# Kernel optimization log

Measured on AMD Instinct MI355X. Metric: run time of the kernel, lower is better.

The kernel has to match this reference:

```python
import jax, jax.numpy as jnp
import numpy as np

MIN = 1e-15
EPS = 1e-6

# ---- Poincare-ball (c=1) helpers (hyrnn-style MobiusGRU / MobiusLinear) ----

def _artanh(x):
    x = jnp.clip(x, -1 + 1e-7, 1 - 1e-7)
    return 0.5 * (jnp.log1p(x) - jnp.log1p(-x))

def _norm(x):
    return jnp.sqrt(jnp.maximum(jnp.sum(x * x, -1, keepdims=True), MIN))

def m_add(x, y):
    x2 = jnp.sum(x * x, -1, keepdims=True)
    y2 = jnp.sum(y * y, -1, keepdims=True)
    xy = jnp.sum(x * y, -1, keepdims=True)
    num = (1 + 2 * xy + y2) * x + (1 - x2) * y
    den = 1 + 2 * xy + x2 * y2
    return num / jnp.maximum(den, MIN)

def m_matvec(M, x):
    xn = _norm(x)
    mx = x @ M.T
    mxn = _norm(mx)
    return jnp.tanh(mxn / xn * _artanh(xn)) * mx / mxn

def m_pw(w, x):
    xn = _norm(x)
    mx = w * x
    mxn = _norm(mx)
    return jnp.tanh(mxn / xn * _artanh(xn)) * mx / mxn

def logmap0(x):
    xn = _norm(x)
    return _artanh(xn) * x / xn

def one_transform(W, h, U, x, b):
    return m_add(m_add(m_matvec(W, h), m_matvec(U, x)), b)

def mobius_gru(xs, Wih, Whh, b):
    # xs: [S, B, I]; Wih/Whh: [3, H, *]; b: [3, H]; chunk order (r, h, z)
    def step(h, x):
        z = jax.nn.sigmoid(logmap0(one_transform(Whh[2], h, Wih[2], x, b[2])))
        r = jax.nn.sigmoid(logmap0(one_transform(Whh[0], h, Wih[0], x, b[0])))
        rh = m_pw(r, h)
        htil = one_transform(Whh[1], rh, Wih[1], x, b[1])
        hn = m_add(h, m_pw(z, m_add(-h, htil)))
        return hn, hn
    h0 = jnp.zeros((xs.shape[1], Whh.shape[1]), xs.dtype)
    _, ys = jax.lax.scan(step, h0, xs)
    return ys

# ---- Lorentz-model helpers ----

def arcosh(x):
    return jnp.log(x) + jnp.log1p(jnp.sqrt(jnp.maximum(x * x - 1 + EPS, 0.0)) / x)

def lorentz_activation(x):
    r = jnp.sqrt(jnp.sum(x * x, -1, keepdims=True))
    return jnp.concatenate([x / r * jnp.sinh(r), jnp.cosh(r)], -1)

def lorentz_to_klein(x):
    return x[..., :-1] / jnp.clip(x[..., -1:], EPS, 1e16)

def poincare_to_lorentz(x):
    r2 = jnp.sum(x * x, -1, keepdims=True)
    return jnp.concatenate([2 * x, 1 + r2], -1) / (1 - r2 + EPS)

# ---- HyperbolicPostAttention ----

def post_attention(x, Wih_f, Whh_f, b_f, Wih_b, Whh_b, b_b, centroid, Wp, bp, beta):
    # x: [L, 100]
    x = x / jnp.sqrt(1 + jnp.sum(x * x, -1, keepdims=True))
    S = x.shape[0] // 100
    f1 = mobius_gru(x.reshape(S, 100, 100), Wih_f, Whh_f, b_f)
    f2 = mobius_gru(x[::-1].reshape(S, 100, 100), Wih_b, Whh_b, b_b)
    f = jnp.concatenate([f1, f2], -1)                       # [S,100,200]
    out_k = lorentz_to_klein(poincare_to_lorentz(f))        # [S,100,200]
    att = m_add(m_matvec(Wp, f), bp)                        # MobiusLinear
    att_l = poincare_to_lorentz(att)                        # [S,100,201]
    cent = lorentz_activation(centroid[None, None, :])      # [1,1,201]
    prod = att_l * cent
    pm = jnp.clip(-jnp.sum(prod[..., :-1], -1) + prod[..., -1], 1.0 + EPS, 1e16)
    a = -beta * arcosh(pm) - 1.0                            # [S,100]; c=1.0
    e = jnp.exp(a - a.max())
    inv_gamma = 1 - jnp.sum(out_k * out_k, -1)
    gamma = jnp.clip(1 / jnp.sqrt(jnp.clip(inv_gamma, EPS, 1 - EPS)), 1 + EPS, 1e16)
    r = e * gamma
    r = r / jnp.sum(r, axis=0)
    o = jnp.einsum('sb,sbd->sd', r, out_k)                  # [S,200]
    return o / (1 + jnp.sqrt(1 + jnp.sum(o * o, -1, keepdims=True)))


def setup_inputs() -> dict:
    key = jax.random.key(0)
    ks = jax.random.split(key, 16)
    n = lambda k, s, sd: jax.random.normal(k, s, jnp.float32) * sd
    return {
        'x_': n(ks[0], (16, 2000, 768), 1.0),
        'W1': n(ks[1], (100, 768), 0.02), 'b1': n(ks[2], (100,), 0.02),
        'W2': n(ks[3], (768, 200), 0.02), 'b2': n(ks[4], (768,), 0.02),
        'Wih_f': n(ks[5], (3, 100, 100), 0.02), 'Whh_f': n(ks[6], (3, 100, 100), 0.02),
        'bias_f': n(ks[7], (3, 100), 0.01),
        'Wih_b': n(ks[8], (3, 100, 100), 0.02), 'Whh_b': n(ks[9], (3, 100, 100), 0.02),
        'bias_b': n(ks[10], (3, 100), 0.01),
        'centroid': n(ks[11], (200,), 0.05),
        'Wp': n(ks[12], (200, 200), 0.02), 'bp': n(ks[13], (200,), 0.01),
        'beta': n(ks[14], (1,), 0.05),
    }


def reference(x_, W1, b1, W2, b2, Wih_f, Whh_f, bias_f, Wih_b, Whh_b, bias_b,
              centroid, Wp, bp, beta):
    xk = lorentz_to_klein(lorentz_activation(x_))           # [N,L,768]

    def per(x):
        h = x @ W1.T + b1                                   # [L,100]
        s = post_attention(h, Wih_f, Whh_f, bias_f, Wih_b, Whh_b, bias_b,
                           centroid, Wp, bp, beta)          # [S,200]
        return s @ W2.T + b2                                # [S,768]

    return jnp.squeeze(jax.vmap(per)(xk))                   # [N,S,768]
```

## Files before the change

### kernel.cpp

```cpp
#include <hip/hip_runtime.h>
#include <hip/hip_bf16.h>

#define MINF 1e-15f
#define EPSF 1e-6f

#define OFF_P    0u
#define OFF_UX   3200000u
#define OFF_WT4  22400000u
#define OFF_F    22460000u
#define OFF_CL   28860000u
#define OFF_A    28860256u
#define OFF_G    28892256u
#define OFF_WGT  28924256u
#define OFF_WI4  OFF_F
#define OFF_W1P  (OFF_F + 60000u)
#define OFF_MX   OFF_UX
#define OFF_WP4  OFF_A
#define OFF_NUB  OFF_P

#define K3_LDS_BYTES ((30000 + 2*13*112) * 4)
#define K2_LDS_BYTES ((3200 + 64*26)*16 + 64*4)
#define K4G_LDS_BYTES ((3200 + 64*26)*16)

__device__ __forceinline__ float wred(float v) {
#pragma unroll
  for (int m = 32; m > 0; m >>= 1) v += __shfl_xor(v, m, 64);
  return v;
}
__device__ __forceinline__ float wredmax(float v) {
#pragma unroll
  for (int m = 32; m > 0; m >>= 1) v = fmaxf(v, __shfl_xor(v, m, 64));
  return v;
}

__device__ __forceinline__ float rcp_(float x) { return __builtin_amdgcn_rcpf(x); }
__device__ __forceinline__ float sqrt_(float x) { return __builtin_amdgcn_sqrtf(x); }
__device__ __forceinline__ float rsq_(float x) { return __builtin_amdgcn_rsqf(x); }
__device__ __forceinline__ float tanh_f(float y) {
  if (y > 15.f) return 1.f;
  float y2 = y * y;
  if (y < 0.1f) return y * (1.f - y2 * (1.f / 3.f) + y2 * y2 * (2.f / 15.f));
  float e = __expf(2.f * y);
  return (e - 1.f) * rcp_(e + 1.f);
}
__device__ __forceinline__ float artanh_ov(float x) {
  x = fminf(x, 1.f - 1e-7f);
  float x2 = x * x;
  if (x < 0.1f) return 1.f + x2 * (1.f / 3.f) + x2 * x2 * 0.2f;
  return 0.5f * __logf((1.f + x) * rcp_(1.f - x)) * rcp_(x);
}
__device__ __forceinline__ float sigm_f(float x) { return rcp_(1.f + __expf(-x)); }
__device__ __forceinline__ float arcosh_(float x) {
  return logf(x) + log1pf(sqrtf(fmaxf(x * x - 1.f + EPSF, 0.f)) / x);
}

__global__ void k0_pack(const float* __restrict__ whh_f, const float* __restrict__ whh_b,
                        const float* __restrict__ wih_f, const float* __restrict__ wih_b,
                        const float* __restrict__ W1, const float* __restrict__ Wp,
                        const float* __restrict__ centroid,
                        float* __restrict__ wt4, float* __restrict__ wi4,
                        float* __restrict__ w1p, float* __restrict__ wp4,
                        float* __restrict__ cl) {
  __shared__ float sred[4];
  if (blockIdx.x == 925) {
    int t = threadIdx.x;
    float v = (t < 200) ? centroid[t] : 0.f;
    float ps = wred(v * v);
    if ((t & 63) == 0) sred[t >> 6] = ps;
    __syncthreads();
    float r = sqrtf(sred[0] + sred[1] + sred[2] + sred[3]);
    if (t < 200) cl[t] = v / r * sinhf(r);
    if (t == 0) cl[200] = coshf(r);
    return;
  }
  int idx = blockIdx.x * 256 + threadIdx.x;
  if (idx < 60000) {
    int kk = idx & 3; int t = idx >> 2;
    int j = t % 100; t /= 100;
    int k4 = t % 25; t /= 25;
    int g = t % 3; int dir = t / 3;
    const float* src = dir ? whh_b : whh_f;
    wt4[idx] = src[g * 10000 + j * 100 + k4 * 4 + kk];
  } else if (idx < 120000) {
    int i2 = idx - 60000;
    int kk = i2 & 3; int t = i2 >> 2;
    int c = t % 100; t /= 100;
    int k4 = t % 25; t /= 25;
    int g = t % 3; int dir = t / 3;
    const float* src = dir ? wih_b : wih_f;
    wi4[i2] = src[g * 10000 + c * 100 + k4 * 4 + kk];
  } else if (idx < 196800) {
    int i2 = idx - 120000;
    int kk = i2 & 3; int t = i2 >> 2;
    int c = t % 100; int k4 = t / 100;
    w1p[i2] = W1[c * 768 + k4 * 4 + kk];
  } else if (idx < 236800) {
    int i3 = idx - 196800;
    int kk = i3 & 3; int t = i3 >> 2;
    int c = t % 100; int t2 = t / 100;
    int k4 = t2 % 50; int ch = t2 / 50;
    wp4[i3] = Wp[(size_t)(ch * 100 + c) * 200 + k4 * 4 + kk];
  }
}

__global__ __launch_bounds__(256, 2) void k1(const float* __restrict__ x_,
                                             const float* __restrict__ w1p,
                                             const float* __restrict__ b1,
                                             float* __restrict__ p) {
  __shared__ float4 wl[16 * 128];
  __shared__ float4 xl[64 * 16];
  __shared__ float ns[64];
  __shared__ float sscale[64];
  int t = threadIdx.x;
  int row0 = blockIdx.x * 64;
  int cg = t & 31, rg = t >> 5;
  const float4* wsrc = (const float4*)w1p;
  float nacc[4] = {0, 0, 0, 0};
  float acc[8][4] = {};
  for (int kc = 0; kc < 12; kc++) {
    int k0f4 = kc * 16;
    __syncthreads();
#pragma unroll
    for (int q = 0; q < 4; q++) {
      int idx = t + 256 * q;
      int r = idx >> 4, c4 = idx & 15;
      float4 v = *(const float4*)(x_ + (size_t)(row0 + r) * 768 + (size_t)(k0f4 + c4) * 4);
      xl[idx] = v;
      nacc[q] += v.x * v.x + v.y * v.y + v.z * v.z + v.w * v.w;
    }
#pragma unroll
    for (int q = 0; q < 8; q++) {
      int idx = t + 256 * q;
      int k4 = idx >> 7, c = idx & 127;
      float4 v = {0, 0, 0, 0};
      if (c < 100) v = wsrc[(size_t)(k0f4 + k4) * 100 + c];
      wl[idx] = v;
    }
    __syncthreads();
#pragma unroll 4
    for (int k4 = 0; k4 < 16; k4++) {
      float4 wv[4];
#pragma unroll
      for (int j = 0; j < 4; j++) wv[j] = wl[k4 * 128 + cg + 32 * j];
#pragma unroll
      for (int i = 0; i < 8; i++) {
        float4 pv = xl[(rg * 8 + i) * 16 + k4];
#pragma unroll
        for (int j = 0; j < 4; j++)
          acc[i][j] += pv.x * wv[j].x + pv.y * wv[j].y + pv.z * wv[j].z + pv.w * wv[j].w;
      }
    }
  }
  __syncthreads();
#pragma unroll
  for (int q = 0; q < 4; q++) {
    float v = nacc[q];
#pragma unroll
    for (int m = 8; m > 0; m >>= 1) v += __shfl_xor(v, m, 64);
    if ((t & 15) == 0) ns[(t >> 4) + 16 * q] = v;
  }
  __syncthreads();
  if (t < 64) {
    float rr = sqrt_(fmaxf(ns[t], MINF));
    sscale[t] = tanh_f(rr) * rcp_(rr);
  }
  __syncthreads();
  float bcol[4];
#pragma unroll
  for (int j = 0; j < 4; j++) {
    int col = cg + 32 * j;
    bcol[j] = (col < 100) ? b1[col] : 0.f;
  }
#pragma unroll
  for (int i = 0; i < 8; i++) {
    int r = rg * 8 + i;
    float s = sscale[r];
    float hv[4]; float ss = 0.f;
#pragma unroll
    for (int j = 0; j < 4; j++) {
      int col = cg + 32 * j;
      hv[j] = (col < 100) ? (s * acc[i][j] + bcol[j]) : 0.f;
      ss += hv[j] * hv[j];
    }
#pragma unroll
    for (int m = 16; m > 0; m >>= 1) ss += __shfl_xor(ss, m, 64);
    float inv = rsq_(1.f + ss);
    float* prow = p + (size_t)(row0 + r) * 100;
#pragma unroll
    for (int j = 0; j < 4; j++) {
      int col = cg + 32 * j;
      if (col < 100) prow[col] = hv[j] * inv;
    }
  }
}

__global__ __launch_bounds__(256, 2) void k2(const float* __restrict__ p,
                                             const float* __restrict__ wi4,
                                             float* __restrict__ ux) {
  extern __shared__ float4 l4[];
  float4* wl = l4;
  float4* pl = l4 + 3200;
  float* alx = (float*)(l4 + 3200 + 64 * 26);
  int t = threadIdx.x;
  int bx = blockIdx.x;
  int combo = bx / 500, tile = bx % 500;
  int row0 = tile * 64;
  int cg = t & 31, rg = t >> 5;
  const float4* wsrc = (const float4*)wi4 + (size_t)combo * 2500;
#pragma unroll
  for (int q = 0; q < 13; q++) {
    int idx = t + 256 * q;
    if (idx < 3200) {
      int k4 = idx >> 7, c = idx & 127;
      float4 v = {0, 0, 0, 0};
      if (c < 100) v = wsrc[k4 * 100 + c];
      wl[idx] = v;
    }
  }
  const float4* psrc = (const float4*)(p + (size_t)row0 * 100);
#pragma unroll
  for (int q = 0; q < 7; q++) {
    int idx = t + 256 * q;
    if (idx < 1600) {
      int r = idx / 25, c4 = idx % 25;
      pl[r * 26 + c4] = psrc[idx];
    }
  }
  __syncthreads();
  {
    int w = t >> 6, lane = t & 63;
    const float* pf = (const float*)pl;
    for (int r = w * 16; r < w * 16 + 16; r++) {
      float v0 = pf[r * 104 + lane];
      float v1 = (lane < 36) ? pf[r * 104 + 64 + lane] : 0.f;
      float s2 = wred(v0 * v0 + v1 * v1);
      if (lane == 0) {
        float xn = sqrt_(fmaxf(s2, MINF));
        alx[r] = artanh_ov(xn);
      }
    }
  }
  __syncthreads();
  float acc[8][4] = {};
#pragma unroll 5
  for (int k4 = 0; k4 < 25; k4++) {
    float4 wv[4];
#pragma unroll
    for (int j = 0; j < 4; j++) wv[j] = wl[k4 * 128 + cg + 32 * j];
#pragma unroll
    for (int i = 0; i < 8; i++) {
      float4 pv = pl[(rg * 8 + i) * 26 + k4];
#pragma unroll
      for (int j = 0; j < 4; j++)
        acc[i][j] += pv.x * wv[j].x + pv.y * wv[j].y + pv.z * wv[j].z + pv.w * wv[j].w;
    }
  }
#pragma unroll
  for (int i = 0; i < 8; i++) {
    int r = rg * 8 + i;
    float ss = acc[i][0] * acc[i][0] + acc[i][1] * acc[i][1] +
               acc[i][2] * acc[i][2] + acc[i][3] * acc[i][3];
#pragma unroll
    for (int m = 16; m > 0; m >>= 1) ss += __shfl_xor(ss, m, 64);
    float mxn = sqrt_(fmaxf(ss, MINF));
    float sc = tanh_f(mxn * alx[r]) * rcp_(mxn);
    float* dst = ux + ((size_t)combo * 32000 + row0 + r) * 100;
#pragma unroll
    for (int j = 0; j < 4; j++) {
      int col = cg + 32 * j;
      if (col < 100) dst[col] = sc * acc[i][j];
    }
  }
}

__global__ __launch_bounds__(256) void k2b(const float* __restrict__ ux,
                                           const float* __restrict__ bias_f,
                                           const float* __restrict__ bias_b,
                                           float* __restrict__ nub) {
  int t = threadIdx.x; int w = t >> 6; int lane = t & 63;
  int gr0 = blockIdx.x * 64;
  int combo = gr0 / 32000;
  int dir = combo / 3, g = combo % 3;
  const float* bias = (dir ? bias_b : bias_f) + g * 100;
  float b0 = bias[lane];
  float b1 = (lane < 36) ? bias[64 + lane] : 0.f;
  for (int i = w * 16; i < w * 16 + 16; i++) {
    const float* u = ux + (size_t)(gr0 + i) * 100;
    float u0 = u[lane];
    float u1 = (lane < 36) ? u[64 + lane] : 0.f;
    float n2 = wred(u0 * u0 + u1 * u1);
    float ub = wred(u0 * b0 + u1 * b1);
    if (lane == 0) { nub[gr0 + i] = n2; nub[192000 + gr0 + i] = ub; }
  }
}

__device__ __forceinline__ void mv100x2_reg(const float* __restrict__ Wz,
                                            const float* __restrict__ Wr,
                                            const float* __restrict__ hrow,
                                            int lane, bool hi,
                                            float& mz0, float& mz1,
                                            float& mr0, float& mr1) {
  const float4* Wz4 = (const float4*)Wz;
  const float4* Wr4 = (const float4*)Wr;
  const float4* h4 = (const float4*)hrow;
  float4 az0 = {0, 0, 0, 0}, az1 = {0, 0, 0, 0};
  float4 ar0 = {0, 0, 0, 0}, ar1 = {0, 0, 0, 0};
#pragma unroll 5
  for (int k4 = 0; k4 < 25; k4++) {
    float4 hv = h4[k4];
    float4 wz = Wz4[k4 * 100 + lane];
    float4 wr = Wr4[k4 * 100 + lane];
    az0.x += wz.x * hv.x; az0.y += wz.y * hv.y; az0.z += wz.z * hv.z; az0.w += wz.w * hv.w;
    ar0.x += wr.x * hv.x; ar0.y += wr.y * hv.y; ar0.z += wr.z * hv.z; ar0.w += wr.w * hv.w;
    if (hi) {
      float4 wzh = Wz4[k4 * 100 + 64 + lane];
      float4 wrh = Wr4[k4 * 100 + 64 + lane];
      az1.x += wzh.x * hv.x; az1.y += wzh.y * hv.y; az1.z += wzh.z * hv.z; az1.w += wzh.w * hv.w;
      ar1.x += wrh.x * hv.x; ar1.y += wrh.y * hv.y; ar1.z += wrh.z * hv.z; ar1.w += wrh.w * hv.w;
    }
  }
  mz0 = az0.x + az0.y + az0.z + az0.w;
  mr0 = ar0.x + ar0.y + ar0.z + ar0.w;
  mz1 = az1.x + az1.y + az1.z + az1.w;
  mr1 = ar1.x + ar1.y + ar1.z + ar1.w;
}

__device__ __forceinline__ void mv100_reg(const float* __restrict__ Wg,
                                          const float* __restrict__ hrow,
                                          int lane, bool hi,
                                          float& m0, float& m1) {
  const float4* W4 = (const float4*)Wg;
  const float4* h4 = (const float4*)hrow;
  float4 a0 = {0, 0, 0, 0}, a1 = {0, 0, 0, 0};
#pragma unroll 5
  for (int k4 = 0; k4 < 25; k4++) {
    float4 hv = h4[k4];
    float4 w0 = W4[k4 * 100 + lane];
    a0.x += w0.x * hv.x; a0.y += w0.y * hv.y; a0.z += w0.z * hv.z; a0.w += w0.w * hv.w;
    if (hi) {
      float4 w1 = W4[k4 * 100 + 64 + lane];
      a1.x += w1.x * hv.x; a1.y += w1.y * hv.y; a1.z += w1.z * hv.z; a1.w += w1.w * hv.w;
    }
  }
  m0 = a0.x + a0.y + a0.z + a0.w;
  m1 = a1.x + a1.y + a1.z + a1.w;
}

__device__ __forceinline__ void gate_ot(float m0, float m1, float u0, float u1,
                                        float b0v, float b1v, float C, float ub, float nb2,
                                        float alphah,
                                        float& c0, float& c1, float& Fout) {
  float A = wred(m0 * m0 + m1 * m1);
  float B = wred(m0 * u0 + m1 * u1);
  float Mb = wred(m0 * b0v + m1 * b1v);
  float mxn = sqrt_(fmaxf(A, MINF));
  float gam = tanh_f(mxn * alphah) * rcp_(mxn);
  float x2 = gam * gam * A, xy = gam * B;
  float rd = rcp_(fmaxf(1.f + 2.f * xy + x2 * C, MINF));
  float cA = (1.f + 2.f * xy + C) * gam * rd, cB = (1.f - x2) * rd;
  float D = fmaxf(cA * cA * A + 2.f * cA * cB * B + cB * cB * C, 0.f);
  float E = cA * Mb + cB * ub;
  float r2 = rcp_(fmaxf(1.f + 2.f * E + D * nb2, MINF));
  float t1 = (1.f + 2.f * E + nb2) * r2, t2 = (1.f - D) * r2;
  c0 = t1 * (cA * m0 + cB * u0) + t2 * b0v;
  c1 = t1 * (cA * m1 + cB * u1) + t2 * b1v;
  Fout = fmaxf(t1 * t1 * D + 2.f * t1 * t2 * E + t2 * t2 * nb2, MINF);
}

__global__ __launch_bounds__(1024, 1) void k3(const float* __restrict__ ux,
                                              const float* __restrict__ nub,
                                              const float* __restrict__ wt4,
                                              const float* __restrict__ bias_f,
                                              const float* __restrict__ bias_b,
                                              float* __restrict__ f) {
  extern __shared__ float lds[];
  float* Wlds = lds;
  float* hl = lds + 30000;
  float* rhl = hl + 13 * 112;
  int t = threadIdx.x; int w = t >> 6; int lane = t & 63;
  bool hi = lane < 36;
  int bx = blockIdx.x;
  int grp = bx >> 3; int blki = bx & 7;
  int n = grp >> 1; int dir = grp & 1;
  int b0 = blki * 13; int nrows = min(13, 100 - b0);
  const float* bias = dir ? bias_b : bias_f;
  const float4* wsrc4 = (const float4*)(wt4 + dir * 30000);
  float4* Wlds4 = (float4*)Wlds;
#pragma unroll
  for (int q = 0; q < 8; q++) { int idx = t + 1024 * q; if (idx < 7500) Wlds4[idx] = wsrc4[idx]; }
  int row = w; bool erow = (w < nrows);
  if (erow) {
    hl[row * 112 + lane] = 0.f;
    if (hi) hl[row * 112 + 64 + lane] = 0.f;
  }
  __syncthreads();
  if (!erow) return;

  int b = b0 + row;
  float nh2 = 0.f, h0 = 0.f, h1 = 0.f;
  float br0 = bias[lane],       br1 = hi ? bias[64 + lane] : 0.f;
  float bh0 = bias[100 + lane], bh1 = hi ? bias[164 + lane] : 0.f;
  float bz0 = bias[200 + lane], bz1 = hi ? bias[264 + lane] : 0.f;
  float nbr2 = wred(br0 * br0 + br1 * br1);
  float nbh2 = wred(bh0 * bh0 + bh1 * bh1);
  float nbz2 = wred(bz0 * bz0 + bz1 * bz1);

  for (int s = 0; s < 20; s++) {
    float mz0, mz1, mr0, mr1;
    mv100x2_reg(Wlds + 2 * 10000, Wlds + 0 * 10000, hl + row * 112, lane, hi,
                mz0, mz1, mr0, mr1);
    int l = dir ? (1999 - (s * 100 + b)) : (s * 100 + b);
    size_t rowg = (size_t)n * 2000 + l;
    size_t iz = (size_t)(dir * 3 + 2) * 32000 + rowg;
    size_t ir = (size_t)(dir * 3 + 0) * 32000 + rowg;
    size_t ih = (size_t)(dir * 3 + 1) * 32000 + rowg;
    const float* uxz = ux + iz * 100;
    const float* uxr = ux + ir * 100;
    const float* uxhp = ux + ih * 100;
    float uz0 = uxz[lane],  uz1 = hi ? uxz[lane + 64] : 0.f;
    float ur0 = uxr[lane],  ur1 = hi ? uxr[lane + 64] : 0.f;
    float uxh0 = uxhp[lane], uxh1 = hi ? uxhp[lane + 64] : 0.f;
    float Cz = nub[iz], ubz = nub[192000 + iz];
    float Cr = nub[ir], ubr = nub[192000 + ir];
    float Ch = nub[ih], ubh = nub[192000 + ih];
    float xnh = sqrt_(fmaxf(nh2, MINF));
    float alphah = artanh_ov(xnh);
    float cz0, cz1, Fz, cr0, cr1, Fr;
    gate_ot(mz0, mz1, uz0, uz1, bz0, bz1, Cz, ubz, nbz2, alphah, cz0, cz1, Fz);
    gate_ot(mr0, mr1, ur0, ur1, br0, br1, Cr, ubr, nbr2, alphah, cr0, cr1, Fr);
    float lgz = artanh_ov(sqrt_(Fz));
    float z0 = sigm_f(lgz * cz0), z1 = sigm_f(lgz * cz1);
    float lgr = artanh_ov(sqrt_(Fr));
    float rg0 = sigm_f(lgr * cr0), rg1 = sigm_f(lgr * cr1);
    float mx0 = rg0 * h0, mx1 = rg1 * h1;
    float G = wred(mx0 * mx0 + mx1 * mx1);
    float mxnr = sqrt_(fmaxf(G, MINF));
    float srh = tanh_f(mxnr * alphah) * rcp_(mxnr);
    rhl[row * 112 + lane] = srh * mx0;
    if (hi) rhl[row * 112 + lane + 64] = srh * mx1;
    float nrh2 = srh * srh * G;
    float mh0, mh1;
    mv100_reg(Wlds + 1 * 10000, rhl + row * 112, lane, hi, mh0, mh1);
    float xnrh = sqrt_(fmaxf(nrh2, MINF));
    float alpharh = artanh_ov(xnrh);
    float ct0, ct1, T;
    gate_ot(mh0, mh1, uxh0, uxh1, bh0, bh1, Ch, ubh, nbh2, alpharh, ct0, ct1, T);
    float U = wred(h0 * ct0 + h1 * ct1);
    float rdd = rcp_(fmaxf(1.f - 2.f * U + nh2 * T, MINF));
    float cAd = (1.f - 2.f * U + T) * rdd, cBd = (1.f - nh2) * rdd;
    float d0 = -cAd * h0 + cBd * ct0, d1 = -cAd * h1 + cBd * ct1;
    float nd2 = fmaxf(cAd * cAd * nh2 - 2.f * cAd * cBd * U + cBd * cBd * T, MINF);
    float zd0 = z0 * d0, zd1 = z1 * d1;
    float P = wred(zd0 * zd0 + zd1 * zd1);
    float Q = wred(h0 * zd0 + h1 * zd1);
    float xnd = sqrt_(nd2);
    float mxnp = sqrt_(fmaxf(P, MINF));
    float sp = tanh_f(mxnp * artanh_ov(xnd)) * rcp_(mxnp);
    float y2p = sp * sp * P, xyp = sp * Q;
    float r3 = rcp_(fmaxf(1.f + 2.f * xyp + nh2 * y2p, MINF));
    float A1 = (1.f + 2.f * xyp + y2p) * r3, B1 = (1.f - nh2) * r3 * sp;
    float hn0 = A1 * h0 + B1 * zd0, hn1 = A1 * h1 + B1 * zd1;
    nh2 = fmaxf(A1 * A1 * nh2 + 2.f * A1 * B1 * Q + B1 * B1 * P, 0.f);
    h0 = hn0; h1 = hn1;
    hl[row * 112 + lane] = hn0;
    if (hi) hl[row * 112 + lane + 64] = hn1;
    float* fd = f + (((size_t)n * 20 + s) * 100 + b) * 200 + dir * 100;
    fd[lane] = hn0;
    if (hi) fd[lane + 64] = hn1;
  }
}

__global__ __launch_bounds__(256, 2) void k4ag(const float* __restrict__ f,
                                               const float* __restrict__ wp4,
                                               float* __restrict__ mx) {
  extern __shared__ float4 g4[];
  float4* wl = g4;
  float4* pl = g4 + 3200;
  int t = threadIdx.x;
  int bx = blockIdx.x;
  int ch = bx & 1, tile = bx >> 1;
  int row0 = tile * 64;
  int cg = t & 31, rg = t >> 5;
  const float4* wsrc = (const float4*)wp4 + (size_t)ch * 5000;
  const float4* psrc = (const float4*)(f + (size_t)row0 * 200);
  float acc[8][4] = {};
  for (int kc = 0; kc < 2; kc++) {
    __syncthreads();
#pragma unroll
    for (int q = 0; q < 13; q++) {
      int idx = t + 256 * q;
      if (idx < 3200) {
        int k4 = idx >> 7, c = idx & 127;
        float4 v = {0, 0, 0, 0};
        if (c < 100) v = wsrc[(kc * 25 + k4) * 100 + c];
        wl[idx] = v;
      }
    }
#pragma unroll
    for (int q = 0; q < 7; q++) {
      int idx = t + 256 * q;
      if (idx < 1600) {
        int r = idx / 25, k4 = idx % 25;
        pl[r * 26 + k4] = psrc[r * 50 + kc * 25 + k4];
      }
    }
    __syncthreads();
#pragma unroll 5
    for (int k4 = 0; k4 < 25; k4++) {
      float4 wv[4];
#pragma unroll
      for (int j = 0; j < 4; j++) wv[j] = wl[k4 * 128 + cg + 32 * j];
#pragma unroll
      for (int i = 0; i < 8; i++) {
        float4 pv = pl[(rg * 8 + i) * 26 + k4];
#pragma unroll
        for (int j = 0; j < 4; j++)
          acc[i][j] += pv.x * wv[j].x + pv.y * wv[j].y + pv.z * wv[j].z + pv.w * wv[j].w;
      }
    }
  }
#pragma unroll
  for (int i = 0; i < 8; i++) {
    float* dst = mx + (size_t)(row0 + rg * 8 + i) * 200 + ch * 100;
#pragma unroll
    for (int j = 0; j < 4; j++) {
      int col = cg + 32 * j;
      if (col < 100) dst[col] = acc[i][j];
    }
  }
}

__global__ __launch_bounds__(256) void k4ae(const float* __restrict__ f,
                                            const float* __restrict__ mx,
                                            const float* __restrict__ bp,
                                            const float* __restrict__ cl,
                                            const float* __restrict__ beta_p,
                                            float* __restrict__ a_out, float* __restrict__ g_out) {
  int t = threadIdx.x; int w = t >> 6; int lane = t & 63;
  int row0 = blockIdx.x * 64;
  float beta = beta_p[0];
  float c200 = cl[200];
  float b_0 = bp[lane], b_1 = bp[lane + 64], b_2 = bp[lane + 128];
  float b_3 = (lane < 8) ? bp[lane + 192] : 0.f;
  float c_0 = cl[lane], c_1 = cl[lane + 64], c_2 = cl[lane + 128];
  float c_3 = (lane < 8) ? cl[lane + 192] : 0.f;
  float nbp2 = wred(b_0 * b_0 + b_1 * b_1 + b_2 * b_2 + b_3 * b_3);
  for (int r = w * 16; r < w * 16 + 16; r++) {
    const float* fr = f + (size_t)(row0 + r) * 200;
    const float* mr = mx + (size_t)(row0 + r) * 200;
    float f0 = fr[lane], f1 = fr[lane + 64], f2 = fr[lane + 128];
    float f3 = (lane < 8) ? fr[lane + 192] : 0.f;
    float nf2 = wred(f0 * f0 + f1 * f1 + f2 * f2 + f3 * f3);
    float xn = sqrt_(fmaxf(nf2, MINF));
    float alx = artanh_ov(xn);
    float m0 = mr[lane], m1 = mr[lane + 64], m2 = mr[lane + 128];
    float m3 = (lane < 8) ? mr[lane + 192] : 0.f;
    float A = wred(m0 * m0 + m1 * m1 + m2 * m2 + m3 * m3);
    float B = wred(m0 * b_0 + m1 * b_1 + m2 * b_2 + m3 * b_3);
    float mxn = sqrt_(fmaxf(A, MINF));
    float gam = tanh_f(mxn * alx) * rcp_(mxn);
    float x2 = gam * gam * A, y2 = nbp2, xy = gam * B;
    float rd = rcp_(fmaxf(1.f + 2.f * xy + x2 * y2, MINF));
    float cA = (1.f + 2.f * xy + y2) * gam * rd, cB = (1.f - x2) * rd;
    float a0 = cA * m0 + cB * b_0, a1 = cA * m1 + cB * b_1;
    float a2 = cA * m2 + cB * b_2, a3 = cA * m3 + cB * b_3;
    float r2 = wred(a0 * a0 + a1 * a1 + a2 * a2 + a3 * a3);
    float dc = wred(a0 * c_0 + a1 * c_1 + a2 * c_2 + a3 * c_3);
    float pm = (-2.f * dc + (1.f + r2) * c200) / (1.f - r2 + EPSF);
    pm = fminf(fmaxf(pm, 1.f + EPSF), 1e16f);
    float av = -beta * arcosh_(pm) - 1.f;
    float invg = 1.f - 4.f * nf2 / ((1.f + nf2) * (1.f + nf2));
    invg = fminf(fmaxf(invg, EPSF), 1.f - EPSF);
    float gv = fminf(fmaxf(rsq_(invg), 1.f + EPSF), 1e16f);
    if (lane == 0) { a_out[row0 + r] = av; g_out[row0 + r] = gv; }
  }
}

__global__ __launch_bounds__(256) void k4b(const float* __restrict__ a_in,
                                           const float* __restrict__ g_in,
                                           float* __restrict__ wgt) {
  __shared__ float rl[2000];
  __shared__ float sred[4];
  __shared__ float rsinv[100];
  int n = blockIdx.x; int t = threadIdx.x;
  int w = t >> 6, lane = t & 63;
  const float* ap = a_in + n * 2000;
  const float* gp = g_in + n * 2000;
  float av[8]; float am = -1e30f;
#pragma unroll
  for (int q = 0; q < 8; q++) {
    int i = t + 256 * q;
    av[q] = (i < 2000) ? ap[i] : -1e30f;
    am = fmaxf(am, av[q]);
  }
  am = wredmax(am);
  if (lane == 0) sred[w] = am;
  __syncthreads();
  float amax = fmaxf(fmaxf(sred[0], sred[1]), fmaxf(sred[2], sred[3]));
#pragma unroll
  for (int q = 0; q < 8; q++) {
    int i = t + 256 * q;
    if (i < 2000) rl[i] = expf(av[q] - amax) * gp[i];
  }
  __syncthreads();
  if (t < 100) {
    float ssum = 0.f;
#pragma unroll
    for (int s = 0; s < 20; s++) ssum += rl[s * 100 + t];
    rsinv[t] = 1.f / ssum;
  }
  __syncthreads();
#pragma unroll
  for (int q = 0; q < 8; q++) {
    int i = t + 256 * q;
    if (i < 2000) wgt[n * 2000 + i] = rl[i] * rsinv[i % 100];
  }
}

__global__ __launch_bounds__(256) void k4c(const float* __restrict__ f, const float* __restrict__ wgt,
                                           const float* __restrict__ W2, const float* __restrict__ b2,
                                           float* __restrict__ out) {
  __shared__ float cw[100];
  __shared__ float part[4][204];
  __shared__ float ol[200];
  __shared__ float sred[4];
  int bx = blockIdx.x; int n = bx / 20, s = bx % 20;
  int t = threadIdx.x; int w = t >> 6; int lane = t & 63;
  const float* fb = f + ((size_t)n * 20 + s) * 100 * 200;
  for (int bi = w * 25; bi < w * 25 + 25; bi++) {
    const float* fr = fb + bi * 200;
    float v0 = fr[lane], v1 = fr[lane + 64], v2 = fr[lane + 128];
    float v3 = (lane < 8) ? fr[lane + 192] : 0.f;
    float s2 = wred(v0 * v0 + v1 * v1 + v2 * v2 + v3 * v3);
    if (lane == 0) cw[bi] = wgt[n * 2000 + s * 100 + bi] * 2.f * rcp_(1.f + s2);
  }
  __syncthreads();
  float o0 = 0, o1 = 0, o2 = 0, o3 = 0;
  for (int bi = w * 25; bi < w * 25 + 25; bi++) {
    float c = cw[bi];
    const float* fr = fb + bi * 200;
    o0 += c * fr[lane]; o1 += c * fr[lane + 64]; o2 += c * fr[lane + 128];
    if (lane < 8) o3 += c * fr[lane + 192];
  }
  part[w][lane] = o0; part[w][lane + 64] = o1; part[w][lane + 128] = o2;
  if (lane < 8) part[w][lane + 192] = o3;
  __syncthreads();
  float o = 0.f;
  if (t < 200) o = part[0][t] + part[1][t] + part[2][t] + part[3][t];
  float ps = (t < 200) ? o * o : 0.f;
  ps = wred(ps);
  if (lane == 0) sred[w] = ps;
  __syncthreads();
  float no2 = sred[0] + sred[1] + sred[2] + sred[3];
  float denom = 1.f + sqrtf(1.f + no2);
  if (t < 200) ol[t] = o / denom;
  __syncthreads();
  const float4* ol4 = (const float4*)ol;
#pragma unroll
  for (int jj = 0; jj < 3; jj++) {
    int j = t + 256 * jj;
    const float4* wrow = (const float4*)(W2 + (size_t)j * 200);
    float a0 = 0, a1 = 0, a2 = 0, a3 = 0;
    for (int k4 = 0; k4 < 50; k4++) {
      float4 wv = wrow[k4]; float4 ov = ol4[k4];
      a0 += wv.x * ov.x; a1 += wv.y * ov.y; a2 += wv.z * ov.z; a3 += wv.w * ov.w;
    }
    out[((size_t)n * 20 + s) * 768 + j] = a0 + a1 + a2 + a3 + b2[j];
  }
}

extern "C" void kernel_launch(void* const* d_in, const int* in_sizes, int n_in,
                              void* d_out, int out_size, void* d_ws, size_t ws_size,
                              hipStream_t stream) {
  const float* x_     = (const float*)d_in[0];
  const float* W1     = (const float*)d_in[1];
  const float* b1     = (const float*)d_in[2];
  const float* W2     = (const float*)d_in[3];
  const float* b2     = (const float*)d_in[4];
  const float* Wih_f  = (const float*)d_in[5];
  const float* Whh_f  = (const float*)d_in[6];
  const float* bias_f = (const float*)d_in[7];
  const float* Wih_b  = (const float*)d_in[8];
  const float* Whh_b  = (const float*)d_in[9];
  const float* bias_b = (const float*)d_in[10];
  const float* centroid = (const float*)d_in[11];
  const float* Wp     = (const float*)d_in[12];
  const float* bp     = (const float*)d_in[13];
  const float* beta   = (const float*)d_in[14];
  float* out = (float*)d_out;
  float* ws = (float*)d_ws;
  float* p   = ws + OFF_P;
  float* ux  = ws + OFF_UX;
  float* wt4 = ws + OFF_WT4;
  float* f   = ws + OFF_F;
  float* wi4 = ws + OFF_WI4;
  float* w1p = ws + OFF_W1P;
  float* mx  = ws + OFF_MX;
  float* wp4 = ws + OFF_WP4;
  float* nub = ws + OFF_NUB;
  float* cl  = ws + OFF_CL;
  float* aa  = ws + OFF_A;
  float* gg  = ws + OFF_G;
  float* wg  = ws + OFF_WGT;

  (void)hipFuncSetAttribute(reinterpret_cast<const void*>(k3),
                            hipFuncAttributeMaxDynamicSharedMemorySize, K3_LDS_BYTES);
  (void)hipFuncSetAttribute(reinterpret_cast<const void*>(k2),
                            hipFuncAttributeMaxDynamicSharedMemorySize, K2_LDS_BYTES);
  (void)hipFuncSetAttribute(reinterpret_cast<const void*>(k4ag),
                            hipFuncAttributeMaxDynamicSharedMemorySize, K4G_LDS_BYTES);

  k0_pack<<<926, 256, 0, stream>>>(Whh_f, Whh_b, Wih_f, Wih_b, W1, Wp, centroid,
                                   wt4, wi4, w1p, wp4, cl);
  k1<<<500, 256, 0, stream>>>(x_, w1p, b1, p);
  k2<<<3000, 256, K2_LDS_BYTES, stream>>>(p, wi4, ux);
  k2b<<<3000, 256, 0, stream>>>(ux, bias_f, bias_b, nub);
  k3<<<256, 1024, K3_LDS_BYTES, stream>>>(ux, nub, wt4, bias_f, bias_b, f);
  k4ag<<<1000, 256, K4G_LDS_BYTES, stream>>>(f, wp4, mx);
  k4ae<<<500, 256, 0, stream>>>(f, mx, bp, cl, beta, aa, gg);
  k4b<<<16, 256, 0, stream>>>(aa, gg, wg);
  k4c<<<320, 256, 0, stream>>>(f, wg, W2, b2, out);
}
```

Baseline: 783.0 us.

## Fuse bias dot-products into GEMM epilogues and replace mx buffer with scalar reductions

The k2 GEMM epilogue now computes the per-row norm and bias dot-product directly and writes them as the nub scalars, removing the separate k2b pass over ux when the workspace is large enough. The k4ag GEMM no longer writes the full 200-wide mx matrix. It reduces each row to the scalars |mx|^2, mx·bp, mx·centroid and |f|^2, and a lightweight k4ael kernel combines them algebraically using precomputed |bp|^2 and bp·centroid. This cuts a full write and re-read of two large intermediates at the cost of extra shuffle reductions and a changed floating-point summation order.

```diff
diff --git a/kernel.cpp b/kernel.cpp
--- a/kernel.cpp
+++ b/kernel.cpp
@@ -12,11 +12,10 @@
 #define OFF_A    28860256u
 #define OFF_G    28892256u
 #define OFF_WGT  28924256u
+#define OFF_NUBT 28956256u
 #define OFF_WI4  OFF_F
 #define OFF_W1P  (OFF_F + 60000u)
-#define OFF_MX   OFF_UX
 #define OFF_WP4  OFF_A
-#define OFF_NUB  OFF_P
 
 #define K3_LDS_BYTES ((30000 + 2*13*112) * 4)
 #define K2_LDS_BYTES ((3200 + 64*26)*16 + 64*4)
@@ -57,20 +56,30 @@
 __global__ void k0_pack(const float* __restrict__ whh_f, const float* __restrict__ whh_b,
                         const float* __restrict__ wih_f, const float* __restrict__ wih_b,
                         const float* __restrict__ W1, const float* __restrict__ Wp,
-                        const float* __restrict__ centroid,
+                        const float* __restrict__ centroid, const float* __restrict__ bp,
                         float* __restrict__ wt4, float* __restrict__ wi4,
                         float* __restrict__ w1p, float* __restrict__ wp4,
                         float* __restrict__ cl) {
-  __shared__ float sred[4];
+  __shared__ float sr1[4], sr2[4], sr3[4];
   if (blockIdx.x == 925) {
-    int t = threadIdx.x;
+    int t = threadIdx.x; int w = t >> 6, lane = t & 63;
     float v = (t < 200) ? centroid[t] : 0.f;
     float ps = wred(v * v);
-    if ((t & 63) == 0) sred[t >> 6] = ps;
+    if (lane == 0) sr1[w] = ps;
     __syncthreads();
-    float r = sqrtf(sred[0] + sred[1] + sred[2] + sred[3]);
-    if (t < 200) cl[t] = v / r * sinhf(r);
+    float r = sqrtf(sr1[0] + sr1[1] + sr1[2] + sr1[3]);
+    float clv = (t < 200) ? (v / r * sinhf(r)) : 0.f;
+    if (t < 200) cl[t] = clv;
     if (t == 0) cl[200] = coshf(r);
+    float bv = (t < 200) ? bp[t] : 0.f;
+    float p2 = wred(bv * bv);
+    float p3 = wred(bv * clv);
+    if (lane == 0) { sr2[w] = p2; sr3[w] = p3; }
+    __syncthreads();
+    if (t == 0) {
+      cl[204] = sr2[0] + sr2[1] + sr2[2] + sr2[3];
+      cl[205] = sr3[0] + sr3[1] + sr3[2] + sr3[3];
+    }
     return;
   }
   int idx = blockIdx.x * 256 + threadIdx.x;
@@ -194,9 +203,13 @@
   }
 }
 
-__global__ __launch_bounds__(256, 2) void k2(const float* __restrict__ p,
-                                             const float* __restrict__ wi4,
-                                             float* __restrict__ ux) {
+template <bool DO_NUB>
+__global__ __launch_bounds__(256, 2) void k2t(const float* __restrict__ p,
+                                              const float* __restrict__ wi4,
+                                              const float* __restrict__ bias_f,
+                                              const float* __restrict__ bias_b,
+                                              float* __restrict__ ux,
+                                              float* __restrict__ nub) {
   extern __shared__ float4 l4[];
   float4* wl = l4;
   float4* pl = l4 + 3200;
@@ -255,15 +268,37 @@
         acc[i][j] += pv.x * wv[j].x + pv.y * wv[j].y + pv.z * wv[j].z + pv.w * wv[j].w;
     }
   }
+  float bcol[4] = {0, 0, 0, 0};
+  if (DO_NUB) {
+    int dir = combo / 3, g = combo % 3;
+    const float* bias = (dir ? bias_b : bias_f) + g * 100;
+#pragma unroll
+    for (int j = 0; j < 4; j++) {
+      int col = cg + 32 * j;
+      bcol[j] = (col < 100) ? bias[col] : 0.f;
+    }
+  }
 #pragma unroll
   for (int i = 0; i < 8; i++) {
     int r = rg * 8 + i;
     float ss = acc[i][0] * acc[i][0] + acc[i][1] * acc[i][1] +
                acc[i][2] * acc[i][2] + acc[i][3] * acc[i][3];
-#pragma unroll
-    for (int m = 16; m > 0; m >>= 1) ss += __shfl_xor(ss, m, 64);
+    float ub = 0.f;
+    if (DO_NUB)
+      ub = acc[i][0] * bcol[0] + acc[i][1] * bcol[1] +
+           acc[i][2] * bcol[2] + acc[i][3] * bcol[3];
+#pragma unroll
+    for (int m = 16; m > 0; m >>= 1) {
+      ss += __shfl_xor(ss, m, 64);
+      if (DO_NUB) ub += __shfl_xor(ub, m, 64);
+    }
     float mxn = sqrt_(fmaxf(ss, MINF));
     float sc = tanh_f(mxn * alx[r]) * rcp_(mxn);
+    if (DO_NUB && cg == 0) {
+      size_t gi = (size_t)combo * 32000 + row0 + r;
+      nub[gi] = sc * sc * ss;
+      nub[192000 + gi] = sc * ub;
+    }
     float* dst = ux + ((size_t)combo * 32000 + row0 + r) * 100;
 #pragma unroll
     for (int j = 0; j < 4; j++) {
@@ -472,7 +507,10 @@
 
 __global__ __launch_bounds__(256, 2) void k4ag(const float* __restrict__ f,
                                                const float* __restrict__ wp4,
-                                               float* __restrict__ mx) {
+                                               const float* __restrict__ bp,
+                                               const float* __restrict__ cl,
+                                               float* __restrict__ Ah, float* __restrict__ Bh,
+                                               float* __restrict__ Mh, float* __restrict__ nf2o) {
   extern __shared__ float4 g4[];
   float4* wl = g4;
   float4* pl = g4 + 3200;
@@ -484,6 +522,7 @@
   const float4* wsrc = (const float4*)wp4 + (size_t)ch * 5000;
   const float4* psrc = (const float4*)(f + (size_t)row0 * 200);
   float acc[8][4] = {};
+  float nfa[8] = {};
   for (int kc = 0; kc < 2; kc++) {
     __syncthreads();
 #pragma unroll
@@ -505,6 +544,13 @@
       }
     }
     __syncthreads();
+    if (cg < 25) {
+#pragma unroll
+      for (int i = 0; i < 8; i++) {
+        float4 v = pl[(rg * 8 + i) * 26 + cg];
+        nfa[i] += v.x * v.x + v.y * v.y + v.z * v.z + v.w * v.w;
+      }
+    }
 #pragma unroll 5
     for (int k4 = 0; k4 < 25; k4++) {
       float4 wv[4];
@@ -519,61 +565,71 @@
       }
     }
   }
+  float bpc[4], clc[4];
+#pragma unroll
+  for (int j = 0; j < 4; j++) {
+    int lc = cg + 32 * j;
+    bool v = lc < 100;
+    bpc[j] = v ? bp[ch * 100 + lc] : 0.f;
+    clc[j] = v ? cl[ch * 100 + lc] : 0.f;
+  }
 #pragma unroll
   for (int i = 0; i < 8; i++) {
-    float* dst = mx + (size_t)(row0 + rg * 8 + i) * 200 + ch * 100;
-#pragma unroll
-    for (int j = 0; j < 4; j++) {
-      int col = cg + 32 * j;
-      if (col < 100) dst[col] = acc[i][j];
-    }
-  }
-}
-
-__global__ __launch_bounds__(256) void k4ae(const float* __restrict__ f,
-                                            const float* __restrict__ mx,
-                                            const float* __restrict__ bp,
-                                            const float* __restrict__ cl,
-                                            const float* __restrict__ beta_p,
-                                            float* __restrict__ a_out, float* __restrict__ g_out) {
-  int t = threadIdx.x; int w = t >> 6; int lane = t & 63;
-  int row0 = blockIdx.x * 64;
+    int r = row0 + rg * 8 + i;
+    float a2 = acc[i][0] * acc[i][0] + acc[i][1] * acc[i][1] +
+               acc[i][2] * acc[i][2] + acc[i][3] * acc[i][3];
+    float ab = acc[i][0] * bpc[0] + acc[i][1] * bpc[1] +
+               acc[i][2] * bpc[2] + acc[i][3] * bpc[3];
+    float ac = acc[i][0] * clc[0] + acc[i][1] * clc[1] +
+               acc[i][2] * clc[2] + acc[i][3] * clc[3];
+    float nf = nfa[i];
+#pragma unroll
+    for (int m = 16; m > 0; m >>= 1) {
+      a2 += __shfl_xor(a2, m, 64);
+      ab += __shfl_xor(ab, m, 64);
+      ac += __shfl_xor(ac, m, 64);
+      nf += __shfl_xor(nf, m, 64);
+    }
+    if (cg == 0) {
+      Ah[ch * 32000 + r] = a2;
+      Bh[ch * 32000 + r] = ab;
+      Mh[ch * 32000 + r] = ac;
+      if (ch == 0) nf2o[r] = nf;
+    }
+  }
+}
+
+__global__ __launch_bounds__(256) void k4ael(const float* __restrict__ Ah,
+                                             const float* __restrict__ Bh,
+                                             const float* __restrict__ Mh,
+                                             const float* __restrict__ nf2a,
+                                             const float* __restrict__ cl,
+                                             const float* __restrict__ beta_p,
+                                             float* __restrict__ a_out,
+                                             float* __restrict__ g_out) {
+  int r = blockIdx.x * 256 + threadIdx.x;
+  float A = Ah[r] + Ah[32000 + r];
+  float B = Bh[r] + Bh[32000 + r];
+  float Mc = Mh[r] + Mh[32000 + r];
+  float nf2 = nf2a[r];
+  float c200 = cl[200], nbp2 = cl[204], bpcl = cl[205];
   float beta = beta_p[0];
-  float c200 = cl[200];
-  float b_0 = bp[lane], b_1 = bp[lane + 64], b_2 = bp[lane + 128];
-  float b_3 = (lane < 8) ? bp[lane + 192] : 0.f;
-  float c_0 = cl[lane], c_1 = cl[lane + 64], c_2 = cl[lane + 128];
-  float c_3 = (lane < 8) ? cl[lane + 192] : 0.f;
-  float nbp2 = wred(b_0 * b_0 + b_1 * b_1 + b_2 * b_2 + b_3 * b_3);
-  for (int r = w * 16; r < w * 16 + 16; r++) {
-    const float* fr = f + (size_t)(row0 + r) * 200;
-    const float* mr = mx + (size_t)(row0 + r) * 200;
-    float f0 = fr[lane], f1 = fr[lane + 64], f2 = fr[lane + 128];
-    float f3 = (lane < 8) ? fr[lane + 192] : 0.f;
-    float nf2 = wred(f0 * f0 + f1 * f1 + f2 * f2 + f3 * f3);
-    float xn = sqrt_(fmaxf(nf2, MINF));
-    float alx = artanh_ov(xn);
-    float m0 = mr[lane], m1 = mr[lane + 64], m2 = mr[lane + 128];
-    float m3 = (lane < 8) ? mr[lane + 192] : 0.f;
-    float A = wred(m0 * m0 + m1 * m1 + m2 * m2 + m3 * m3);
-    float B = wred(m0 * b_0 + m1 * b_1 + m2 * b_2 + m3 * b_3);
-    float mxn = sqrt_(fmaxf(A, MINF));
-    float gam = tanh_f(mxn * alx) * rcp_(mxn);
-    float x2 = gam * gam * A, y2 = nbp2, xy = gam * B;
-    float rd = rcp_(fmaxf(1.f + 2.f * xy + x2 * y2, MINF));
-    float cA = (1.f + 2.f * xy + y2) * gam * rd, cB = (1.f - x2) * rd;
-    float a0 = cA * m0 + cB * b_0, a1 = cA * m1 + cB * b_1;
-    float a2 = cA * m2 + cB * b_2, a3 = cA * m3 + cB * b_3;
-    float r2 = wred(a0 * a0 + a1 * a1 + a2 * a2 + a3 * a3);
-    float dc = wred(a0 * c_0 + a1 * c_1 + a2 * c_2 + a3 * c_3);
-    float pm = (-2.f * dc + (1.f + r2) * c200) / (1.f - r2 + EPSF);
-    pm = fminf(fmaxf(pm, 1.f + EPSF), 1e16f);
-    float av = -beta * arcosh_(pm) - 1.f;
-    float invg = 1.f - 4.f * nf2 / ((1.f + nf2) * (1.f + nf2));
-    invg = fminf(fmaxf(invg, EPSF), 1.f - EPSF);
-    float gv = fminf(fmaxf(rsq_(invg), 1.f + EPSF), 1e16f);
-    if (lane == 0) { a_out[row0 + r] = av; g_out[row0 + r] = gv; }
-  }
+  float alx = artanh_ov(sqrt_(fmaxf(nf2, MINF)));
+  float mxn = sqrt_(fmaxf(A, MINF));
+  float gam = tanh_f(mxn * alx) * rcp_(mxn);
+  float x2 = gam * gam * A, xy = gam * B;
+  float rd = rcp_(fmaxf(1.f + 2.f * xy + x2 * nbp2, MINF));
+  float cA = (1.f + 2.f * xy + nbp2) * gam * rd, cB = (1.f - x2) * rd;
+  float r2 = fmaxf(cA * cA * A + 2.f * cA * cB * B + cB * cB * nbp2, 0.f);
+  float dc = cA * Mc + cB * bpcl;
+  float pm = (-2.f * dc + (1.f + r2) * c200) / (1.f - r2 + EPSF);
+  pm = fminf(fmaxf(pm, 1.f + EPSF), 1e16f);
+  float av = -beta * arcosh_(pm) - 1.f;
+  float invg = 1.f - 4.f * nf2 / ((1.f + nf2) * (1.f + nf2));
+  invg = fminf(fmaxf(invg, EPSF), 1.f - EPSF);
+  float gv = fminf(fmaxf(rsq_(invg), 1.f + EPSF), 1e16f);
+  a_out[r] = av;
+  g_out[r] = gv;
 }
 
 __global__ __launch_bounds__(256) void k4b(const float* __restrict__ a_in,
@@ -695,29 +751,39 @@
   float* f   = ws + OFF_F;
   float* wi4 = ws + OFF_WI4;
   float* w1p = ws + OFF_W1P;
-  float* mx  = ws + OFF_MX;
   float* wp4 = ws + OFF_WP4;
-  float* nub = ws + OFF_NUB;
   float* cl  = ws + OFF_CL;
   float* aa  = ws + OFF_A;
   float* gg  = ws + OFF_G;
   float* wg  = ws + OFF_WGT;
+  float* Ah  = ws + OFF_UX;
+  float* Bh  = ws + OFF_UX + 64000;
+  float* Mh  = ws + OFF_UX + 128000;
+  float* nf2 = ws + OFF_UX + 192000;
+  bool fuse_nub = ws_size >= (size_t)(OFF_NUBT + 384000u) * 4u;
+  float* nub = fuse_nub ? (ws + OFF_NUBT) : (ws + OFF_P);
 
   (void)hipFuncSetAttribute(reinterpret_cast<const void*>(k3),
                             hipFuncAttributeMaxDynamicSharedMemorySize, K3_LDS_BYTES);
-  (void)hipFuncSetAttribute(reinterpret_cast<const void*>(k2),
+  (void)hipFuncSetAttribute(reinterpret_cast<const void*>(k2t<true>),
+                            hipFuncAttributeMaxDynamicSharedMemorySize, K2_LDS_BYTES);
+  (void)hipFuncSetAttribute(reinterpret_cast<const void*>(k2t<false>),
                             hipFuncAttributeMaxDynamicSharedMemorySize, K2_LDS_BYTES);
   (void)hipFuncSetAttribute(reinterpret_cast<const void*>(k4ag),
                             hipFuncAttributeMaxDynamicSharedMemorySize, K4G_LDS_BYTES);
 
-  k0_pack<<<926, 256, 0, stream>>>(Whh_f, Whh_b, Wih_f, Wih_b, W1, Wp, centroid,
+  k0_pack<<<926, 256, 0, stream>>>(Whh_f, Whh_b, Wih_f, Wih_b, W1, Wp, centroid, bp,
                                    wt4, wi4, w1p, wp4, cl);
   k1<<<500, 256, 0, stream>>>(x_, w1p, b1, p);
-  k2<<<3000, 256, K2_LDS_BYTES, stream>>>(p, wi4, ux);
-  k2b<<<3000, 256, 0, stream>>>(ux, bias_f, bias_b, nub);
+  if (fuse_nub) {
+    k2t<true><<<3000, 256, K2_LDS_BYTES, stream>>>(p, wi4, bias_f, bias_b, ux, nub);
+  } else {
+    k2t<false><<<3000, 256, K2_LDS_BYTES, stream>>>(p, wi4, bias_f, bias_b, ux, nullptr);
+    k2b<<<3000, 256, 0, stream>>>(ux, bias_f, bias_b, nub);
+  }
   k3<<<256, 1024, K3_LDS_BYTES, stream>>>(ux, nub, wt4, bias_f, bias_b, f);
-  k4ag<<<1000, 256, K4G_LDS_BYTES, stream>>>(f, wp4, mx);
-  k4ae<<<500, 256, 0, stream>>>(f, mx, bp, cl, beta, aa, gg);
+  k4ag<<<1000, 256, K4G_LDS_BYTES, stream>>>(f, wp4, bp, cl, Ah, Bh, Mh, nf2);
+  k4ael<<<125, 256, 0, stream>>>(Ah, Bh, Mh, nf2, cl, beta, aa, gg);
   k4b<<<16, 256, 0, stream>>>(aa, gg, wg);
   k4c<<<320, 256, 0, stream>>>(f, wg, W2, b2, out);
 }
```

New measurement: 728.3 us. -7.0%, faster.
